# Optimization experiments

Measured on AMD Instinct MI355X. Metric: run time of the kernel, lower is better.

The kernel has to match this reference:

```python
import jax, jax.numpy as jnp
import numpy as np
import math

EPS_LN = 1e-5
EPS_Q = 1e-5


def _layernorm(x):
    # LayerNorm without affine (elementwise_affine=False), biased variance
    mu = jnp.mean(x, axis=-1, keepdims=True)
    var = jnp.var(x, axis=-1, keepdims=True)
    return (x - mu) * jax.lax.rsqrt(var + EPS_LN)


def _quantize_activations(x):
    # per-row 8-bit absmax quantization
    eta = jnp.maximum(jnp.max(jnp.abs(x), axis=-1, keepdims=True), EPS_Q)
    x_q = jnp.clip(jnp.round(x * (127.0 / eta)), -128.0, 127.0)
    return x_q, eta / 127.0


def _quantize_weights(w):
    # absmean ternary quantization
    gamma = jnp.maximum(jnp.mean(jnp.abs(w)), EPS_Q)
    w_q = jnp.round(jnp.clip(w / gamma, -1.0, 1.0))
    return w_q, gamma


def setup_inputs() -> dict:
    key = jax.random.key(0)
    k1, k2 = jax.random.split(key, 2)
    B, S, IN, OUT = 2, 4096, 2048, 8192
    x = jax.random.normal(k1, (B, S, IN), dtype=jnp.float32)
    # kaiming_uniform_(a=sqrt(5)) -> U(-1/sqrt(fan_in), 1/sqrt(fan_in))
    bound = 1.0 / math.sqrt(IN)
    weight = jax.random.uniform(k2, (OUT, IN), dtype=jnp.float32, minval=-bound, maxval=bound)
    bias = jnp.zeros((OUT,), dtype=jnp.float32)
    return {"x": x, "weight": weight, "bias": bias}


def reference(x, weight, bias):
    x_norm = _layernorm(x)
    x_q, x_scale = _quantize_activations(x_norm)      # [B,S,K], [B,S,1]
    w_q, w_scale = _quantize_weights(weight)           # [N,K], scalar
    # int8 GEMM emulated exactly in fp32 (values are small integers, exact)
    out_i = jnp.einsum('bsk,nk->bsn', x_q, w_q)        # int32-equivalent accum
    out = out_i * (w_scale * x_scale) + bias
    return out
```

## Files before the change

### kernel.cpp

```cpp
#include <hip/hip_runtime.h>
#include <stdint.h>

typedef int v4i __attribute__((ext_vector_type(4)));

#define M_DIM 8192
#define N_DIM 8192
#define K_DIM 2048
#define RISKY_TAU 1e-4f
#define BUCKET_CAP 1024
#define SLOT 32768

#define ASYNC16(g, l) __builtin_amdgcn_global_load_lds(                        \
    (const __attribute__((address_space(1))) void*)(uintptr_t)(g),             \
    (__attribute__((address_space(3))) void*)(uint32_t)(uintptr_t)(l), 16, 0, 0)

__global__ __launch_bounds__(256) void abssum_stage1(const float* __restrict__ w,
                                                     float* __restrict__ s1) {
  int b = blockIdx.x * 256 + threadIdx.x;
  const float* p = w + (size_t)b * 128;
  float r[8];
#pragma unroll
  for (int j = 0; j < 8; j++) r[j] = fabsf(p[j]);
  for (int i = 8; i < 128; i += 8) {
#pragma unroll
    for (int j = 0; j < 8; j++) r[j] += fabsf(p[i + j]);
  }
  s1[b] = ((r[0] + r[1]) + (r[2] + r[3])) + ((r[4] + r[5]) + (r[6] + r[7]));
}

__global__ __launch_bounds__(256) void abssum_stage2(const float* __restrict__ s1,
                                                     float* __restrict__ s2) {
  int t = blockIdx.x * 256 + threadIdx.x;
  float v[32];
#pragma unroll
  for (int i = 0; i < 32; i++) v[i] = s1[t * 32 + i];
#pragma unroll
  for (int s = 1; s < 32; s *= 2) {
#pragma unroll
    for (int i = 0; i < 32; i += 2 * s) v[i] += v[i + s];
  }
  s2[t] = v[0];
}

__global__ __launch_bounds__(256) void gamma_stage3(const float* __restrict__ s2,
                                                    float* __restrict__ gp) {
  int t = threadIdx.x;
  float v[16];
#pragma unroll
  for (int i = 0; i < 16; i++) v[i] = s2[t * 16 + i];
#pragma unroll
  for (int s = 1; s < 16; s *= 2) {
#pragma unroll
    for (int i = 0; i < 16; i += 2 * s) v[i] += v[i + s];
  }
  __shared__ float sm[256];
  sm[t] = v[0];
  for (int s = 1; s < 256; s *= 2) {
    __syncthreads();
    if ((t & (2 * s - 1)) == 0) sm[t] += sm[t + s];
  }
  __syncthreads();
  if (t == 0) {
    float g = sm[0] * 0x1p-24f;
    gp[0] = fmaxf(g, 1e-5f);
  }
}

__global__ void zero_counts(int* __restrict__ counts) {
  counts[threadIdx.x] = 0;
}

__global__ __launch_bounds__(256) void wq_kernel(const float4* __restrict__ w4,
                                                 const float* __restrict__ gp,
                                                 int* __restrict__ wq,
                                                 int* __restrict__ counts,
                                                 int* __restrict__ buckets) {
  int i = blockIdx.x * 256 + threadIdx.x;
  float g = gp[0];
  float4 v = w4[i];
  float e[4] = {v.x, v.y, v.z, v.w};
  int q[4];
#pragma unroll
  for (int c = 0; c < 4; c++) {
    q[c] = (int)rintf(fminf(fmaxf(e[c] / g, -1.0f), 1.0f));
    float t = fabsf(e[c]) / g;
    if (fabsf(t - 0.5f) < RISKY_TAU) {
      int flat = i * 4 + c;
      int n = flat >> 11;
      int k = flat & 2047;
      int sgn_neg = (e[c] < 0.0f) ? 1 : 0;
      int sbit = (q[c] == 0) ? sgn_neg : (1 - sgn_neg);
      int b = n >> 7;
      int idx = atomicAdd(&counts[b], 1);
      if (idx < BUCKET_CAP)
        buckets[b * BUCKET_CAP + idx] = k | (n << 11) | (sbit << 24);
    }
  }
  wq[i] = (q[0] & 0xFF) | ((q[1] & 0xFF) << 8) | ((q[2] & 0xFF) << 16) | ((q[3] & 0xFF) << 24);
}

__global__ __launch_bounds__(256) void lnq_kernel(const float* __restrict__ x,
                                                  const float* __restrict__ gp,
                                                  int8_t* __restrict__ xq,
                                                  float* __restrict__ scales) {
  const int row = blockIdx.x;
  const int t = threadIdx.x;
  const float4* xr = (const float4*)(x + (size_t)row * K_DIM);
  float4 a = xr[t];
  float4 b = xr[t + 256];
  double v[8] = {a.x, a.y, a.z, a.w, b.x, b.y, b.z, b.w};
  double s = 0.0, ss = 0.0;
#pragma unroll
  for (int i = 0; i < 8; i++) { s += v[i]; ss += v[i] * v[i]; }
  __shared__ double sm1[256], sm2[256];
  sm1[t] = s; sm2[t] = ss;
  __syncthreads();
  for (int off = 128; off > 0; off >>= 1) {
    if (t < off) { sm1[t] += sm1[t + off]; sm2[t] += sm2[t + off]; }
    __syncthreads();
  }
  double mu = sm1[0] * (1.0 / 2048.0);
  double var = sm2[0] * (1.0 / 2048.0) - mu * mu;
  double inv = 1.0 / sqrt(var + 1e-5);
  __syncthreads();
  double mx = 0.0;
#pragma unroll
  for (int i = 0; i < 8; i++) {
    v[i] = (v[i] - mu) * inv;
    double av = fabs(v[i]);
    if (av > mx) mx = av;
  }
  sm1[t] = mx;
  __syncthreads();
  for (int off = 128; off > 0; off >>= 1) {
    if (t < off) sm1[t] = fmax(sm1[t], sm1[t + off]);
    __syncthreads();
  }
  double eta = fmax(sm1[0], 1e-5);
  double r = 127.0 / eta;
  int q[8];
#pragma unroll
  for (int i = 0; i < 8; i++) {
    double qq = rint(v[i] * r);
    qq = fmin(fmax(qq, -128.0), 127.0);
    q[i] = (int)qq;
  }
  int p0 = (q[0] & 0xFF) | ((q[1] & 0xFF) << 8) | ((q[2] & 0xFF) << 16) | ((q[3] & 0xFF) << 24);
  int p1 = (q[4] & 0xFF) | ((q[5] & 0xFF) << 8) | ((q[6] & 0xFF) << 16) | ((q[7] & 0xFF) << 24);
  int* orow = (int*)(xq + (size_t)row * K_DIM);
  orow[t] = p0;
  orow[t + 256] = p1;
  if (t == 0) scales[row] = (float)((double)gp[0] * eta * (1.0 / 127.0));
}

__global__ __launch_bounds__(512, 2) void gemm_i8_kernel(const int8_t* __restrict__ A,
                                                         const int8_t* __restrict__ B,
                                                         const float* __restrict__ scales,
                                                         const float* __restrict__ bias,
                                                         const int* __restrict__ counts,
                                                         const int* __restrict__ buckets,
                                                         float* __restrict__ C) {
  __shared__ alignas(16) int8_t lds[2 * SLOT];
  const int tid = threadIdx.x;
  const int wave = tid >> 6;
  const int lane = tid & 63;

  const int b = blockIdx.x;
  const int tr = (b & 7) * 4 + ((b >> 3) & 3);
  const int tc = b >> 5;
  const int brow = tr * 256;
  const int bcol = tc * 256;

  const int chunkr = lane >> 2;
  const int sl = lane & 3;
  const int8_t* gA[2];
  const int8_t* gB[2];
  int dA[2], dB[2];
#pragma unroll
  for (int c = 0; c < 2; c++) {
    int ch = wave * 2 + c;
    int r = ch * 16 + chunkr;
    int scol = ((sl ^ ((r >> 1) & 3)) << 4);
    gA[c] = A + (size_t)(brow + r) * K_DIM + scol;
    gB[c] = B + (size_t)(bcol + r) * K_DIM + scol;
    dA[c] = ch * 1024;
    dB[c] = 16384 + ch * 1024;
  }

  const int wr = wave >> 2;
  const int wc = wave & 3;
  const int ks = lane >> 4;
  int aoff[8], boff[4];
#pragma unroll
  for (int m = 0; m < 8; m++) {
    int r = wr * 128 + m * 16 + (lane & 15);
    aoff[m] = r * 64 + ((ks ^ ((r >> 1) & 3)) << 4);
  }
#pragma unroll
  for (int n = 0; n < 4; n++) {
    int r = wc * 64 + n * 16 + (lane & 15);
    boff[n] = 16384 + r * 64 + ((ks ^ ((r >> 1) & 3)) << 4);
  }

  v4i acc[8][4];
  const v4i vzero = {0, 0, 0, 0};
#pragma unroll
  for (int m = 0; m < 8; m++)
#pragma unroll
    for (int n = 0; n < 4; n++) acc[m][n] = vzero;

#pragma unroll
  for (int c = 0; c < 2; c++) {
    ASYNC16(gA[c], lds + dA[c]);
    ASYNC16(gB[c], lds + dB[c]);
  }
  __syncthreads();

  int cur = 0;
  for (int t = 0; t < 32; ++t) {
    if (t < 31) {
      const int kt = (t + 1) * 64;
      const int sb = (cur ^ 1) * SLOT;
#pragma unroll
      for (int c = 0; c < 2; c++) {
        ASYNC16(gA[c] + kt, lds + sb + dA[c]);
        ASYNC16(gB[c] + kt, lds + sb + dB[c]);
      }
    }
    const int rb = cur * SLOT;
    v4i bf[4], af[8];
#pragma unroll
    for (int n = 0; n < 4; n++) bf[n] = *(const v4i*)(lds + rb + boff[n]);
#pragma unroll
    for (int m = 0; m < 8; m++) af[m] = *(const v4i*)(lds + rb + aoff[m]);
    __builtin_amdgcn_s_setprio(1);
#pragma unroll
    for (int m = 0; m < 8; m++)
#pragma unroll
      for (int n = 0; n < 4; n++)
        acc[m][n] = __builtin_amdgcn_mfma_i32_16x16x64_i8(af[m], bf[n], acc[m][n], 0, 0, 0);
    __builtin_amdgcn_s_setprio(0);
    __syncthreads();
    cur ^= 1;
  }

#pragma unroll
  for (int m = 0; m < 8; m++)
#pragma unroll
    for (int n = 0; n < 4; n++) acc[m][n] = acc[m][n] + acc[m][n];

  const int crow0 = brow + wr * 128;
  const int ccol0 = bcol + wc * 64;

#define CORR(J)                                                                \
  {                                                                            \
    _Pragma("unroll") for (int m = 0; m < 8; m++) {                            \
      _Pragma("unroll") for (int r = 0; r < 4; r++) {                          \
        int grow = crow0 + m * 16 + ((lane >> 4) << 2) + r;                    \
        int xv = (int)A[(size_t)grow * K_DIM + k];                             \
        acc[m][J][r] += sv * xv;                                               \
      }                                                                        \
    }                                                                          \
  }

  {
    int bkt = (bcol + wc * 64) >> 7;
    int cnt = counts[bkt];
    if (cnt > BUCKET_CAP) cnt = BUCKET_CAP;
    const int* bk = buckets + bkt * BUCKET_CAP;
    for (int e = 0; e < cnt; ++e) {
      int word = bk[e];
      int k = word & 2047;
      int nc = (word >> 11) & 8191;
      int sv = ((word >> 24) & 1) ? -1 : 1;
      if (((nc >> 6) & 1) == (wc & 1) && (nc & 15) == (lane & 15)) {
        int j = (nc >> 4) & 3;
        switch (j) {
          case 0: CORR(0); break;
          case 1: CORR(1); break;
          case 2: CORR(2); break;
          case 3: CORR(3); break;
        }
      }
    }
  }
#undef CORR

#pragma unroll
  for (int m = 0; m < 8; m++) {
#pragma unroll
    for (int r = 0; r < 4; r++) {
      int grow = crow0 + m * 16 + ((lane >> 4) << 2) + r;
      float sc = scales[grow] * 0.5f;
      float* crow = C + (size_t)grow * N_DIM;
#pragma unroll
      for (int n = 0; n < 4; n++) {
        int gcol = ccol0 + n * 16 + (lane & 15);
        crow[gcol] = (float)acc[m][n][r] * sc + bias[gcol];
      }
    }
  }
}

extern "C" void kernel_launch(void* const* d_in, const int* in_sizes, int n_in,
                              void* d_out, int out_size, void* d_ws, size_t ws_size,
                              hipStream_t stream) {
  const float* x = (const float*)d_in[0];
  const float* w = (const float*)d_in[1];
  const float* bias = (const float*)d_in[2];
  float* out = (float*)d_out;

  char* ws = (char*)d_ws;
  float* s1 = (float*)(ws);
  float* s2 = (float*)(ws + 0x100000);
  float* gamma_f = (float*)(ws + 0x110000);
  float* scales = (float*)(ws + 0x120000);
  int* counts = (int*)(ws + 0x130000);
  int* buckets = (int*)(ws + 0x131000);
  int8_t* Aq = (int8_t*)(ws + 0x200000);
  int8_t* Wq = (int8_t*)(ws + 0x200000 + (size_t)M_DIM * K_DIM);

  abssum_stage1<<<512, 256, 0, stream>>>(w, s1);
  abssum_stage2<<<16, 256, 0, stream>>>(s1, s2);
  gamma_stage3<<<1, 256, 0, stream>>>(s2, gamma_f);
  zero_counts<<<1, 64, 0, stream>>>(counts);
  wq_kernel<<<(N_DIM * K_DIM / 4 + 255) / 256, 256, 0, stream>>>(
      (const float4*)w, gamma_f, (int*)Wq, counts, buckets);
  lnq_kernel<<<M_DIM, 256, 0, stream>>>(x, gamma_f, Aq, scales);
  gemm_i8_kernel<<<1024, 512, 0, stream>>>(Aq, Wq, scales, bias, counts, buckets, out);
}
```

Baseline: 287.0 us.

## Stream A tiles into registers and triple-buffer B in LDS

The A operand no longer goes through LDS. Each wave loads its own A fragments straight from global memory into a double-buffered register array one k-step ahead. B keeps using async global-to-LDS copies, now with three 16KB LDS slots, prefetching two steps ahead and synchronised with explicit vmcnt waits plus raw barriers instead of __syncthreads. This halves LDS usage and aims to hide load latency better. The cost is that A rows are fetched redundantly by the four column waves, and the extra register arrays raise VGPR pressure, which may cause spills under the 512x2 launch bound.

```diff
diff --git a/kernel.cpp b/kernel.cpp
--- a/kernel.cpp
+++ b/kernel.cpp
@@ -8,7 +8,7 @@
 #define K_DIM 2048
 #define RISKY_TAU 1e-4f
 #define BUCKET_CAP 1024
-#define SLOT 32768
+#define BSLOT 16384
 
 #define ASYNC16(g, l) __builtin_amdgcn_global_load_lds(                        \
     (const __attribute__((address_space(1))) void*)(uintptr_t)(g),             \
@@ -160,7 +160,7 @@
                                                          const int* __restrict__ counts,
                                                          const int* __restrict__ buckets,
                                                          float* __restrict__ C) {
-  __shared__ alignas(16) int8_t lds[2 * SLOT];
+  __shared__ alignas(16) int8_t lds[3 * BSLOT];
   const int tid = threadIdx.x;
   const int wave = tid >> 6;
   const int lane = tid & 63;
@@ -173,34 +173,28 @@
 
   const int chunkr = lane >> 2;
   const int sl = lane & 3;
-  const int8_t* gA[2];
   const int8_t* gB[2];
-  int dA[2], dB[2];
+  int dB[2];
 #pragma unroll
   for (int c = 0; c < 2; c++) {
     int ch = wave * 2 + c;
     int r = ch * 16 + chunkr;
     int scol = ((sl ^ ((r >> 1) & 3)) << 4);
-    gA[c] = A + (size_t)(brow + r) * K_DIM + scol;
     gB[c] = B + (size_t)(bcol + r) * K_DIM + scol;
-    dA[c] = ch * 1024;
-    dB[c] = 16384 + ch * 1024;
+    dB[c] = ch * 1024;
   }
 
   const int wr = wave >> 2;
   const int wc = wave & 3;
   const int ks = lane >> 4;
-  int aoff[8], boff[4];
-#pragma unroll
-  for (int m = 0; m < 8; m++) {
-    int r = wr * 128 + m * 16 + (lane & 15);
-    aoff[m] = r * 64 + ((ks ^ ((r >> 1) & 3)) << 4);
-  }
+  int boff[4];
 #pragma unroll
   for (int n = 0; n < 4; n++) {
     int r = wc * 64 + n * 16 + (lane & 15);
-    boff[n] = 16384 + r * 64 + ((ks ^ ((r >> 1) & 3)) << 4);
-  }
+    boff[n] = r * 64 + ((ks ^ ((r >> 1) & 3)) << 4);
+  }
+
+  const int8_t* gAr = A + (size_t)(brow + wr * 128 + (lane & 15)) * K_DIM + ks * 16;
 
   v4i acc[8][4];
   const v4i vzero = {0, 0, 0, 0};
@@ -209,40 +203,51 @@
 #pragma unroll
     for (int n = 0; n < 4; n++) acc[m][n] = vzero;
 
-#pragma unroll
-  for (int c = 0; c < 2; c++) {
-    ASYNC16(gA[c], lds + dA[c]);
-    ASYNC16(gB[c], lds + dB[c]);
-  }
-  __syncthreads();
-
-  int cur = 0;
-  for (int t = 0; t < 32; ++t) {
-    if (t < 31) {
-      const int kt = (t + 1) * 64;
-      const int sb = (cur ^ 1) * SLOT;
-#pragma unroll
-      for (int c = 0; c < 2; c++) {
-        ASYNC16(gA[c] + kt, lds + sb + dA[c]);
-        ASYNC16(gB[c] + kt, lds + sb + dB[c]);
-      }
-    }
-    const int rb = cur * SLOT;
-    v4i bf[4], af[8];
-#pragma unroll
-    for (int n = 0; n < 4; n++) bf[n] = *(const v4i*)(lds + rb + boff[n]);
-#pragma unroll
-    for (int m = 0; m < 8; m++) af[m] = *(const v4i*)(lds + rb + aoff[m]);
-    __builtin_amdgcn_s_setprio(1);
-#pragma unroll
-    for (int m = 0; m < 8; m++)
-#pragma unroll
-      for (int n = 0; n < 4; n++)
-        acc[m][n] = __builtin_amdgcn_mfma_i32_16x16x64_i8(af[m], bf[n], acc[m][n], 0, 0, 0);
-    __builtin_amdgcn_s_setprio(0);
-    __syncthreads();
-    cur ^= 1;
-  }
+  v4i aA[8], aB[8], bf[4];
+
+#pragma unroll
+  for (int c = 0; c < 2; c++) ASYNC16(gB[c], lds + dB[c]);
+#pragma unroll
+  for (int m = 0; m < 8; m++) aA[m] = *(const v4i*)(gAr + (size_t)m * 16 * K_DIM);
+#pragma unroll
+  for (int c = 0; c < 2; c++) ASYNC16(gB[c] + 64, lds + BSLOT + dB[c]);
+  asm volatile("s_waitcnt vmcnt(2)" ::: "memory");
+  __builtin_amdgcn_s_barrier();
+
+  int rbase = 0;
+  int sbase = 2 * BSLOT;
+
+#define GEMM_STEP(T, USE, LOADARR)                                             \
+  {                                                                            \
+    if ((T) < 31) {                                                            \
+      const size_t ka = (size_t)((T) + 1) * 64;                                \
+      _Pragma("unroll") for (int m = 0; m < 8; m++)                            \
+        LOADARR[m] = *(const v4i*)(gAr + (size_t)m * 16 * K_DIM + ka);         \
+    }                                                                          \
+    if ((T) < 30) {                                                            \
+      const int kb = ((T) + 2) * 64;                                           \
+      ASYNC16(gB[0] + kb, lds + sbase + dB[0]);                                \
+      ASYNC16(gB[1] + kb, lds + sbase + dB[1]);                                \
+    }                                                                          \
+    _Pragma("unroll") for (int n = 0; n < 4; n++)                              \
+      bf[n] = *(const v4i*)(lds + rbase + boff[n]);                            \
+    __builtin_amdgcn_s_setprio(1);                                             \
+    _Pragma("unroll") for (int m = 0; m < 8; m++)                              \
+      _Pragma("unroll") for (int n = 0; n < 4; n++)                            \
+        acc[m][n] = __builtin_amdgcn_mfma_i32_16x16x64_i8(USE[m], bf[n], acc[m][n], 0, 0, 0); \
+    __builtin_amdgcn_s_setprio(0);                                             \
+    if ((T) < 30) asm volatile("s_waitcnt vmcnt(2)" ::: "memory");             \
+    else          asm volatile("s_waitcnt vmcnt(0)" ::: "memory");             \
+    __builtin_amdgcn_s_barrier();                                              \
+    rbase = (rbase == 2 * BSLOT) ? 0 : rbase + BSLOT;                          \
+    sbase = (sbase == 2 * BSLOT) ? 0 : sbase + BSLOT;                          \
+  }
+
+  for (int tt = 0; tt < 16; ++tt) {
+    GEMM_STEP(tt * 2, aA, aB)
+    GEMM_STEP(tt * 2 + 1, aB, aA)
+  }
+#undef GEMM_STEP
 
 #pragma unroll
   for (int m = 0; m < 8; m++)
```

Result: slower. 455.7 us (+58.8%).
